# Kernel optimization log

Hardware: AMD Instinct MI355X
Metric: run time of the kernel (lower is better)

## Reference

```python
import jax, jax.numpy as jnp
import numpy as np
from jax import lax

EPS = 1e-5
B, T, H, L, K = 64, 1024, 12, 120, 5  # batch, seq len, hidden, lstm layers, conv kernel


def _init(key, shape, scale):
    return scale * jax.random.normal(key, shape, dtype=jnp.float32)


def setup_inputs() -> dict:
    key = jax.random.key(0)
    ks = jax.random.split(key, 16)
    return {
        "x": jax.random.normal(ks[0], (B, 6, T), dtype=jnp.float32),
        "conv_acc_w": _init(ks[1], (6, 6, K), 0.3),
        "conv_acc_b": jnp.zeros((6,), jnp.float32),
        "bn1_gamma": jnp.ones((6,), jnp.float32),
        "bn1_beta": jnp.zeros((6,), jnp.float32),
        "conv_ang_w": _init(ks[2], (6, 6, K), 0.3),
        "conv_ang_b": jnp.zeros((6,), jnp.float32),
        "bn2_gamma": jnp.ones((6,), jnp.float32),
        "bn2_beta": jnp.zeros((6,), jnp.float32),
        "attn_w": _init(ks[3], (H, 6), 0.4),
        "attn_b": jnp.zeros((H,), jnp.float32),
        "lstm_wih": _init(ks[4], (L, 4 * H, H), 0.2),
        "lstm_whh": _init(ks[5], (L, 4 * H, H), 0.2),
        "lstm_bih": _init(ks[6], (L, 4 * H), 0.1),
        "lstm_bhh": _init(ks[7], (L, 4 * H), 0.1),
        "lin1_w": _init(ks[8], (H, H), 0.3),
        "lin1_b": jnp.zeros((H,), jnp.float32),
        "lin2_w": _init(ks[9], (H, H), 0.3),
        "lin2_b": jnp.zeros((H,), jnp.float32),
        "mu_w": _init(ks[10], (H, H), 0.3),
        "mu_b": jnp.zeros((H,), jnp.float32),
        "sigma_w": _init(ks[11], (H, H), 0.3),
        "sigma_b": jnp.zeros((H,), jnp.float32),
    }


def _conv1d(x, w, b):
    # x: (B, C, T) valid conv, matches nn.Conv1d
    y = lax.conv_general_dilated(x, w, (1,), "VALID", dimension_numbers=("NCH", "OIH", "NCH"))
    return y + b[None, :, None]


def _batchnorm(x, gamma, beta):
    # training-mode BatchNorm1d: biased batch stats over (N, T)
    mean = jnp.mean(x, axis=(0, 2), keepdims=True)
    var = jnp.var(x, axis=(0, 2), keepdims=True)
    return (x - mean) * lax.rsqrt(var + EPS) * gamma[None, :, None] + beta[None, :, None]


def _lstm_stack(seq_tbh, wih, whh, bias):
    # seq_tbh: (T', B, H); stacked 120-layer LSTM, torch gate order (i, f, g, o)
    b = seq_tbh.shape[1]
    h0 = jnp.zeros((b, H), seq_tbh.dtype)

    def layer(seq, p):
        w_ih, w_hh, bb = p

        def step(carry, xt):
            h, c = carry
            g = xt @ w_ih.T + h @ w_hh.T + bb  # (B, 4H)
            i, f, gg, o = jnp.split(g, 4, axis=-1)
            c_new = jax.nn.sigmoid(f) * c + jax.nn.sigmoid(i) * jnp.tanh(gg)
            h_new = jax.nn.sigmoid(o) * jnp.tanh(c_new)
            return (h_new, c_new), h_new

        (h_T, _), out = lax.scan(step, (h0, h0), seq)
        return out, h_T

    _, h_last = lax.scan(layer, seq_tbh, (wih, whh, bias))
    return h_last  # (L, B, H): final hidden state of every layer


def _forward(x, conv_acc_w, conv_acc_b, bn1_gamma, bn1_beta, conv_ang_w, conv_ang_b,
             bn2_gamma, bn2_beta, attn_w, attn_b, lstm_wih, lstm_whh, lstm_bih, lstm_bhh,
             lin1_w, lin1_b, lin2_w, lin2_b, mu_w, mu_b, sigma_w, sigma_b):
    out_acc = jax.nn.relu(_batchnorm(_conv1d(x, conv_acc_w, conv_acc_b), bn1_gamma, bn1_beta))
    out_ang = jax.nn.relu(_batchnorm(_conv1d(out_acc, conv_ang_w, conv_ang_b), bn2_gamma, bn2_beta))
    feat = jax.nn.relu(jnp.einsum("bct,hc->bth", out_ang, attn_w) + attn_b)  # (B, T-8, H)
    seq = jnp.transpose(feat, (1, 0, 2))  # (T', B, H) time-major for scan
    h_last = _lstm_stack(seq, lstm_wih, lstm_whh, lstm_bih + lstm_bhh)
    h = jnp.transpose(h_last, (1, 0, 2))  # (B, L, H) == hidden_state.permute(1,0,2)
    h = jax.nn.relu(h @ lin1_w.T + lin1_b)
    out = jax.nn.relu(h @ lin2_w.T + lin2_b)
    mu = out @ mu_w.T + mu_b
    log_var = jax.nn.softplus(out @ sigma_w.T + sigma_b)
    return out, mu, log_var


def reference(x, conv_acc_w, conv_acc_b, bn1_gamma, bn1_beta, conv_ang_w, conv_ang_b,
              bn2_gamma, bn2_beta, attn_w, attn_b, lstm_wih, lstm_whh, lstm_bih, lstm_bhh,
              lin1_w, lin1_b, lin2_w, lin2_b, mu_w, mu_b, sigma_w, sigma_b):
    return _forward(x, conv_acc_w, conv_acc_b, bn1_gamma, bn1_beta, conv_ang_w, conv_ang_b,
                    bn2_gamma, bn2_beta, attn_w, attn_b, lstm_wih, lstm_whh, lstm_bih, lstm_bhh,
                    lin1_w, lin1_b, lin2_w, lin2_b, mu_w, mu_b, sigma_w, sigma_b)
```

## Files before the change

kernel.cpp:

```cpp
#include <hip/hip_runtime.h>
#include <math.h>

#define NLAY 120
#define TT   1016
#define NB   64
#define RB   8
#define IRS  32
#define TPB  384
#define BIGF (1 << 20)

typedef float v2f __attribute__((ext_vector_type(2)));

__device__ __forceinline__ float fast_rcp(float x) { return __builtin_amdgcn_rcpf(x); }
__device__ __forceinline__ float fast_sig(float x) { return fast_rcp(1.f + __expf(-x)); }
__device__ __forceinline__ float fast_tanh(float x) { return 1.f - 2.f * fast_rcp(1.f + __expf(2.f * x)); }

__device__ __forceinline__ int poll_ge_ag(const int* p, int tgt, int cur) {
  long g = 0;
  while (cur < tgt) {
    cur = __hip_atomic_load(p, __ATOMIC_RELAXED, __HIP_MEMORY_SCOPE_AGENT);
    if (cur >= tgt) break;
    __builtin_amdgcn_s_sleep(1);
    if (++g > 400000L) break;
  }
  return cur;
}
__device__ __forceinline__ int poll_ge_wg(const int* p, int tgt, int cur) {
  long g = 0;
  while (cur < tgt) {
    cur = __hip_atomic_load(p, __ATOMIC_RELAXED, __HIP_MEMORY_SCOPE_WORKGROUP);
    if (cur >= tgt) break;
    __builtin_amdgcn_s_sleep(1);
    if (++g > 400000L) break;
  }
  return cur;
}

__global__ void k_conv(const float* __restrict__ xin, const float* __restrict__ cw,
                       const float* __restrict__ cb, const float* __restrict__ aff,
                       float* __restrict__ yout, float* __restrict__ stat,
                       int Tin, int Tout, int use_aff)
{
  const int bx = blockIdx.x;
  const int b = bx / 6, co = bx - b * 6;
  const int tid = threadIdx.x;
  __shared__ float wsh[30];
  __shared__ float ssh[6], shsh[6];
  if (tid < 30) wsh[tid] = cw[co * 30 + tid];
  if (tid < 6) {
    ssh[tid]  = use_aff ? aff[tid] : 1.f;
    shsh[tid] = use_aff ? aff[6 + tid] : 0.f;
  }
  __syncthreads();
  const float bias = cb[co];
  float lsum = 0.f, lsq = 0.f;
  for (int t = tid; t < Tout; t += 256) {
    float acc = bias;
#pragma unroll
    for (int ci = 0; ci < 6; ++ci) {
      const float* xr = xin + ((size_t)b * 6 + ci) * Tin + t;
      const float s = ssh[ci], sh = shsh[ci];
#pragma unroll
      for (int k = 0; k < 5; ++k) {
        float v = xr[k];
        if (use_aff) v = fmaxf(fmaf(s, v, sh), 0.f);
        acc += wsh[ci * 5 + k] * v;
      }
    }
    yout[((size_t)b * 6 + co) * Tout + t] = acc;
    lsum += acc; lsq += acc * acc;
  }
  __shared__ float rs[256], rq[256];
  rs[tid] = lsum; rq[tid] = lsq;
  __syncthreads();
  for (int s = 128; s > 0; s >>= 1) {
    if (tid < s) { rs[tid] += rs[tid + s]; rq[tid] += rq[tid + s]; }
    __syncthreads();
  }
  if (tid == 0) { atomicAdd(&stat[co], rs[0]); atomicAdd(&stat[6 + co], rq[0]); }
}

__global__ void k_finalize(const float* __restrict__ stat,
                           const float* __restrict__ gamma, const float* __restrict__ beta,
                           float* __restrict__ aff, float invN)
{
  const int c = threadIdx.x;
  if (c < 6) {
    float mean = stat[c] * invN;
    float var  = stat[6 + c] * invN - mean * mean;
    float sc   = gamma[c] * rsqrtf(var + 1e-5f);
    aff[c]     = sc;
    aff[6 + c] = fmaf(-mean, sc, beta[c]);
  }
}

__global__ void k_attn(const float* __restrict__ y2, const float* __restrict__ aff2,
                       const float* __restrict__ aw, const float* __restrict__ ab,
                       float* __restrict__ seq0)
{
  const int t = blockIdx.x;
  const int tid = threadIdx.x;
  __shared__ float zb[6 * 64];
  if (tid < 384) {
    const int c = tid >> 6, bb = tid & 63;
    float v = y2[((size_t)bb * 6 + c) * TT + t];
    zb[c * 64 + bb] = fmaxf(fmaf(aff2[c], v, aff2[6 + c]), 0.f);
  }
  __syncthreads();
  const int b = tid / 12, j = tid - b * 12;
  float acc = ab[j];
#pragma unroll
  for (int c = 0; c < 6; ++c) acc += aw[j * 6 + c] * zb[c * 64 + b];
  seq0[(size_t)t * 768 + tid] = fmaxf(acc, 0.f);
}

__global__ __launch_bounds__(TPB, 2) void k_lstm(
    const float* __restrict__ wih, const float* __restrict__ whh,
    const float* __restrict__ bih, const float* __restrict__ bhh,
    const float* __restrict__ seq0, float* __restrict__ ring,
    int* __restrict__ prog, int* __restrict__ cons,
    float* __restrict__ hfin)
{
  const int bid  = blockIdx.x;
  const int c    = bid >> 2;
  const int seg  = bid & 3;
  const int tid  = threadIdx.x;
  const int w    = tid >> 6;
  const int lane = tid & 63;
  const int p    = lane / 12;
  const int j    = lane - p * 12;
  const bool act = (p < 5);
  const int pc   = act ? p : 0;
  const int l    = seg * 30 + w * 5 + pc;

  __shared__ __align__(16) float hloc[6][2][64];
  __shared__ __align__(16) float iring[5][IRS][12];
  __shared__ __align__(16) float xring[2][16][12];
  __shared__ __align__(16) float oring[16][12];
  __shared__ int pflag[6];
  __shared__ int cflag[8];
  float* xrf = &xring[0][0][0];

  if (tid < 6) pflag[tid] = 0;
  if (tid < 8) cflag[tid] = 0;
  hloc[w][0][lane] = 0.f; hloc[w][1][lane] = 0.f;
  __syncthreads();

  v2f wx_if[12], wx_go[12], wh_if[12], wh_go[12];
  v2f b_if = (v2f){0.f, 0.f}, b_go = (v2f){0.f, 0.f};
  if (act) {
    const float* wi = wih + l * 576;
    const float* wh = whh + l * 576;
#pragma unroll
    for (int k = 0; k < 12; ++k) {
      wx_if[k] = (v2f){ wi[(j     ) * 12 + k], wi[(j + 12) * 12 + k] };
      wx_go[k] = (v2f){ wi[(j + 24) * 12 + k], wi[(j + 36) * 12 + k] };
      wh_if[k] = (v2f){ wh[(j     ) * 12 + k], wh[(j + 12) * 12 + k] };
      wh_go[k] = (v2f){ wh[(j + 24) * 12 + k], wh[(j + 36) * 12 + k] };
    }
    const float* ba = bih + l * 48;
    const float* bb = bhh + l * 48;
    b_if = (v2f){ ba[j]      + bb[j],      ba[j + 12] + bb[j + 12] };
    b_go = (v2f){ ba[j + 24] + bb[j + 24], ba[j + 36] + bb[j + 36] };
  }

  const int hop_in  = c * 3 + seg - 1;
  const int hop_out = c * 3 + seg;
  const float* rin  = ring + (size_t)((seg > 0) ? hop_in : 0) * (RB * 192);
  float*       rout = ring + (size_t)((seg < 3) ? hop_out : 0) * (RB * 192);
  const bool is_feeder = (w == 0);
  const bool is_tailer = (w == 5) && (seg < 3);

  const int f0 = lane, f1 = lane + 64, f2 = lane + 128;
  const int s0o0 = (f0 / 12) * 768 + (f0 % 12);
  const int s0o1 = (f1 / 12) * 768 + (f1 % 12);
  const int s0o2 = (f2 / 12) * 768 + (f2 % 12);

  auto ld_batch = [&](int m, float* d) {
    if (seg == 0) {
      const float* b = seq0 + (size_t)m * 16 * 768 + c * 12;
      d[0] = b[s0o0]; d[1] = b[s0o1]; d[2] = b[s0o2];
    } else {
      const float* b = rin + (m & (RB - 1)) * 192;
      d[0] = __hip_atomic_load(b + f0, __ATOMIC_RELAXED, __HIP_MEMORY_SCOPE_AGENT);
      d[1] = __hip_atomic_load(b + f1, __ATOMIC_RELAXED, __HIP_MEMORY_SCOPE_AGENT);
      d[2] = __hip_atomic_load(b + f2, __ATOMIC_RELAXED, __HIP_MEMORY_SCOPE_AGENT);
    }
  };

  float pend[3] = {0.f, 0.f, 0.f};
  int kp = 0, kcons = 0;
  if (is_feeder) {
    if (seg > 0) kp = poll_ge_ag(&prog[hop_in], 2, 0);
    float cur[3];
    ld_batch(0, cur);
    ld_batch(1, pend);
    xrf[f0] = cur[0]; xrf[f1] = cur[1]; xrf[f2] = cur[2];
  }

  float cst = 0.f;
  int pcache = 0, ccache = 0;

  auto step = [&](int s, bool guard) __attribute__((always_inline)) {
    const int t  = s - pc;
    const int rb = (s & 1) ^ 1, wb = s & 1;

    const float* ax;
    if (p == 0) ax = (w == 0) ? (xrf + ((s >> 4) & 1) * 192 + (s & 15) * 12)
                              : (&iring[w - 1][s & (IRS - 1)][0]);
    else        ax = &hloc[w][rb][(pc == 0 ? 0 : pc - 1) * 12];
    const float* ah = &hloc[w][rb][pc * 12];

    float4 xA = ((const float4*)ax)[0], xB = ((const float4*)ax)[1], xC = ((const float4*)ax)[2];
    float4 hA = ((const float4*)ah)[0], hB = ((const float4*)ah)[1], hC = ((const float4*)ah)[2];
    float xv[12] = {xA.x,xA.y,xA.z,xA.w, xB.x,xB.y,xB.z,xB.w, xC.x,xC.y,xC.z,xC.w};
    float hv[12] = {hA.x,hA.y,hA.z,hA.w, hB.x,hB.y,hB.z,hB.w, hC.x,hC.y,hC.z,hC.w};

    v2f axif = (v2f){0.f,0.f}, axgo = (v2f){0.f,0.f};
    v2f ahif = b_if, ahgo = b_go;
#pragma unroll
    for (int k = 0; k < 12; ++k) {
      v2f xx = { xv[k], xv[k] };
      axif = __builtin_elementwise_fma(wx_if[k], xx, axif);
      axgo = __builtin_elementwise_fma(wx_go[k], xx, axgo);
    }
#pragma unroll
    for (int k = 0; k < 12; ++k) {
      v2f hh = { hv[k], hv[k] };
      ahif = __builtin_elementwise_fma(wh_if[k], hh, ahif);
      ahgo = __builtin_elementwise_fma(wh_go[k], hh, ahgo);
    }
    v2f aif = axif + ahif, ago = axgo + ahgo;
    float ig = fast_sig(aif.x);
    float fg = fast_sig(aif.y);
    float gg = fast_tanh(ago.x);
    float og = fast_sig(ago.y);

    if (!guard) {
      cst = fg * cst + ig * gg;
      float hn = og * fast_tanh(cst);
      hloc[w][wb][p * 12 + j] = hn;
      if (p == 4) {
        if (w < 5) iring[w][t & (IRS - 1)][j] = hn;
        else if (seg < 3) oring[t & 15][j] = hn;
      }
    } else {
      const bool run = act && (t >= 0) && (t < TT);
      if (run) {
        cst = fg * cst + ig * gg;
        float hn = og * fast_tanh(cst);
        hloc[w][wb][p * 12 + j] = hn;
        if (p == 4) {
          if (w < 5) iring[w][t & (IRS - 1)][j] = hn;
          else if (seg < 3) oring[t & 15][j] = hn;
        }
        if (t == TT - 1) hfin[l * 768 + c * 12 + j] = hn;
      }
    }

    if (is_tailer) {
      const int t4 = s - 4;
      if (t4 >= 0 && t4 < TT && (((t4 & 15) == 15) || t4 == TT - 1)) {
        const int m4 = t4 >> 4;
        if (kcons < m4 - (RB - 1) + 1)
          kcons = poll_ge_ag(&cons[hop_out], m4 - RB + 1, kcons);
        const float* orf = &oring[0][0];
        float o0 = orf[f0], o1 = orf[f1], o2 = orf[f2];
        float* d = rout + (m4 & (RB - 1)) * 192;
        __hip_atomic_store(d + f0, o0, __ATOMIC_RELAXED, __HIP_MEMORY_SCOPE_AGENT);
        __hip_atomic_store(d + f1, o1, __ATOMIC_RELAXED, __HIP_MEMORY_SCOPE_AGENT);
        __hip_atomic_store(d + f2, o2, __ATOMIC_RELAXED, __HIP_MEMORY_SCOPE_AGENT);
        if (lane == 0)
          __hip_atomic_store(&prog[hop_out], m4 + 1, __ATOMIC_RELEASE, __HIP_MEMORY_SCOPE_AGENT);
      }
    }
  };

  for (int s4 = 0; s4 < 1024; s4 += 4) {
    if (is_feeder && (s4 & 15) == 0) {
      const int m = s4 >> 4;
      if (m + 1 < NB) {
        float* xd = xrf + ((m + 1) & 1) * 192;
        xd[f0] = pend[0]; xd[f1] = pend[1]; xd[f2] = pend[2];
      }
      if (m + 2 < NB) {
        if (seg > 0 && kp < m + 3) kp = poll_ge_ag(&prog[hop_in], m + 3, kp);
        ld_batch(m + 2, pend);
      }
      if (seg > 0 && lane == 0)
        __hip_atomic_store(&cons[hop_in], m, __ATOMIC_RELAXED, __HIP_MEMORY_SCOPE_AGENT);
    }

    if (w > 0 && s4 < TT) {
      const int tgt = (s4 + 4 < TT) ? (s4 + 4) : TT;
      if (pcache < tgt) {
        pcache = poll_ge_wg(&pflag[w - 1], tgt, pcache);
        asm volatile("" ::: "memory");
      }
    }
    if (w < 5 && s4 >= 36) {
      const int tgt = s4 - 32;
      if (ccache < tgt) {
        ccache = poll_ge_wg(&cflag[w + 1], tgt, ccache);
        asm volatile("" ::: "memory");
      }
    }

    if (s4 >= 4 && s4 < 1012) {
      step(s4 + 0, false); step(s4 + 1, false); step(s4 + 2, false); step(s4 + 3, false);
    } else {
      step(s4 + 0, true);  step(s4 + 1, true);  step(s4 + 2, true);  step(s4 + 3, true);
    }

    if (lane == 0) {
      asm volatile("" ::: "memory");
      if (w < 5)
        __hip_atomic_store(&pflag[w], s4, __ATOMIC_RELAXED, __HIP_MEMORY_SCOPE_WORKGROUP);
      if (w > 0 && s4 + 3 < TT)
        __hip_atomic_store(&cflag[w], s4 + 4, __ATOMIC_RELAXED, __HIP_MEMORY_SCOPE_WORKGROUP);
    }
  }

  if (lane == 0) {
    asm volatile("" ::: "memory");
    if (w < 5) __hip_atomic_store(&pflag[w], BIGF, __ATOMIC_RELAXED, __HIP_MEMORY_SCOPE_WORKGROUP);
    if (w > 0) __hip_atomic_store(&cflag[w], BIGF, __ATOMIC_RELAXED, __HIP_MEMORY_SCOPE_WORKGROUP);
    if (is_feeder && seg > 0)
      __hip_atomic_store(&cons[hop_in], BIGF, __ATOMIC_RELAXED, __HIP_MEMORY_SCOPE_AGENT);
  }
}

__global__ void k_head(const float* __restrict__ hfin,
                       const float* __restrict__ w1, const float* __restrict__ b1,
                       const float* __restrict__ w2, const float* __restrict__ b2,
                       const float* __restrict__ wm, const float* __restrict__ bm,
                       const float* __restrict__ wsg, const float* __restrict__ bsg,
                       float* __restrict__ out)
{
  const int tid = threadIdx.x;
  __shared__ float s1[144], s2[144], sm[144], ss[144];
  __shared__ float v1[12], v2[12], vm[12], vs[12];
  if (tid < 144) { s1[tid] = w1[tid]; s2[tid] = w2[tid]; sm[tid] = wm[tid]; ss[tid] = wsg[tid]; }
  if (tid < 12)  { v1[tid] = b1[tid]; v2[tid] = b2[tid]; vm[tid] = bm[tid]; vs[tid] = bsg[tid]; }
  __syncthreads();
  const int r = blockIdx.x * 256 + tid;
  const int b = r / 120, l = r - b * 120;
  float h[12];
#pragma unroll
  for (int k = 0; k < 12; ++k) h[k] = hfin[l * 768 + b * 12 + k];
  float u1[12];
#pragma unroll
  for (int u = 0; u < 12; ++u) {
    float a = v1[u];
#pragma unroll
    for (int k = 0; k < 12; ++k) a += s1[u * 12 + k] * h[k];
    u1[u] = fmaxf(a, 0.f);
  }
  float u2[12];
#pragma unroll
  for (int u = 0; u < 12; ++u) {
    float a = v2[u];
#pragma unroll
    for (int k = 0; k < 12; ++k) a += s2[u * 12 + k] * u1[k];
    u2[u] = fmaxf(a, 0.f);
  }
  const size_t base = (size_t)r * 12;
#pragma unroll
  for (int u = 0; u < 12; ++u) out[base + u] = u2[u];
#pragma unroll
  for (int u = 0; u < 12; ++u) {
    float a = vm[u];
#pragma unroll
    for (int k = 0; k < 12; ++k) a += sm[u * 12 + k] * u2[k];
    out[92160 + base + u] = a;
  }
#pragma unroll
  for (int u = 0; u < 12; ++u) {
    float a = vs[u];
#pragma unroll
    for (int k = 0; k < 12; ++k) a += ss[u * 12 + k] * u2[k];
    out[184320 + base + u] = fmaxf(a, 0.f) + log1pf(expf(-fabsf(a)));
  }
}

extern "C" void kernel_launch(void* const* d_in, const int* in_sizes, int n_in,
                              void* d_out, int out_size, void* d_ws, size_t ws_size,
                              hipStream_t stream)
{
  const float* x   = (const float*)d_in[0];
  const float* c1w = (const float*)d_in[1];
  const float* c1b = (const float*)d_in[2];
  const float* g1  = (const float*)d_in[3];
  const float* be1 = (const float*)d_in[4];
  const float* c2w = (const float*)d_in[5];
  const float* c2b = (const float*)d_in[6];
  const float* g2  = (const float*)d_in[7];
  const float* be2 = (const float*)d_in[8];
  const float* aw  = (const float*)d_in[9];
  const float* ab  = (const float*)d_in[10];
  const float* wih = (const float*)d_in[11];
  const float* whh = (const float*)d_in[12];
  const float* bih = (const float*)d_in[13];
  const float* bhh = (const float*)d_in[14];
  const float* l1w = (const float*)d_in[15];
  const float* l1b = (const float*)d_in[16];
  const float* l2w = (const float*)d_in[17];
  const float* l2b = (const float*)d_in[18];
  const float* muw = (const float*)d_in[19];
  const float* mub = (const float*)d_in[20];
  const float* sgw = (const float*)d_in[21];
  const float* sgb = (const float*)d_in[22];

  float* ws    = (float*)d_ws;
  float* stat1 = ws;
  float* stat2 = ws + 12;
  float* aff1  = ws + 24;
  float* aff2  = ws + 36;
  int*   prog  = (int*)(ws + 64);
  int*   cons  = (int*)(ws + 304);
  float* y1    = ws + 576;
  float* y2    = y1 + 391680;
  float* seq0  = y2 + 390144;
  float* ring  = seq0 + 780288;
  float* hfin  = ring + (size_t)192 * RB * 192;

  hipMemsetAsync(d_ws, 0, 576 * sizeof(float), stream);

  k_conv<<<384, 256, 0, stream>>>(x, c1w, c1b, nullptr, y1, stat1, 1024, 1020, 0);
  k_finalize<<<1, 64, 0, stream>>>(stat1, g1, be1, aff1, 1.f / 65280.f);
  k_conv<<<384, 256, 0, stream>>>(y1, c2w, c2b, aff1, y2, stat2, 1020, 1016, 1);
  k_finalize<<<1, 64, 0, stream>>>(stat2, g2, be2, aff2, 1.f / 65024.f);
  k_attn<<<1016, 768, 0, stream>>>(y2, aff2, aw, ab, seq0);
  k_lstm<<<256, TPB, 0, stream>>>(wih, whh, bih, bhh, seq0, ring, prog, cons, hfin);
  k_head<<<30, 256, 0, stream>>>(hfin, l1w, l1b, l2w, l2b, muw, mub, sgw, sgb, (float*)d_out);
}
```

Measured before the change: 811.2 us.

## Process two batch chains per LSTM block with reorganized weight layout and batched flushes

Each LSTM workgroup now runs two batch columns (chains A and B) at once, so half as many blocks are launched and every weight register is reused for two independent recurrences. Gate weights are regrouped into per-gate rows with paired k elements, which lets the input vectors feed packed FMAs directly without broadcasting. The step loop is unrolled by 8 instead of 4, intra-block flag syncs are coarsened, and the output ring flush moves from per-step inside the tail wave to a separate double-buffered flush. The intent is to interleave two dependency chains to hide latency and halve synchronization overhead per sample, at the cost of more registers and LDS per block, and fewer blocks to spread across CUs.

```diff
diff --git a/kernel.cpp b/kernel.cpp
--- a/kernel.cpp
+++ b/kernel.cpp
@@ -7,7 +7,6 @@
 #define RB   8
 #define IRS  32
 #define TPB  384
-#define BIGF (1 << 20)
 
 typedef float v2f __attribute__((ext_vector_type(2)));
 
@@ -122,8 +121,9 @@
     float* __restrict__ hfin)
 {
   const int bid  = blockIdx.x;
-  const int c    = bid >> 2;
+  const int cb   = bid >> 2;
   const int seg  = bid & 3;
+  const int cA   = cb * 2, cB = cb * 2 + 1;
   const int tid  = threadIdx.x;
   const int w    = tid >> 6;
   const int lane = tid & 63;
@@ -133,52 +133,52 @@
   const int pc   = act ? p : 0;
   const int l    = seg * 30 + w * 5 + pc;
 
-  __shared__ __align__(16) float hloc[6][2][64];
-  __shared__ __align__(16) float iring[5][IRS][12];
-  __shared__ __align__(16) float xring[2][16][12];
-  __shared__ __align__(16) float oring[16][12];
-  __shared__ int pflag[6];
-  __shared__ int cflag[8];
-  float* xrf = &xring[0][0][0];
-
-  if (tid < 6) pflag[tid] = 0;
-  if (tid < 8) cflag[tid] = 0;
-  hloc[w][0][lane] = 0.f; hloc[w][1][lane] = 0.f;
+  __shared__ __align__(16) float hlocA[6][2][64], hlocB[6][2][64];
+  __shared__ __align__(16) float iringA[5][IRS][12], iringB[5][IRS][12];
+  __shared__ __align__(16) float xrA[2][192], xrB[2][192];
+  __shared__ __align__(16) float obA[2][192], obB[2][192];
+  __shared__ int pflag[8], cflag[8];
+
+  if (tid < 8) { pflag[tid] = 0; cflag[tid] = 0; }
+  hlocA[w][0][lane] = 0.f; hlocA[w][1][lane] = 0.f;
+  hlocB[w][0][lane] = 0.f; hlocB[w][1][lane] = 0.f;
   __syncthreads();
 
-  v2f wx_if[12], wx_go[12], wh_if[12], wh_go[12];
-  v2f b_if = (v2f){0.f, 0.f}, b_go = (v2f){0.f, 0.f};
+  v2f wx[4][6] = {}, wh2[4][6] = {};
+  float bias[4] = {0.f, 0.f, 0.f, 0.f};
   if (act) {
     const float* wi = wih + l * 576;
     const float* wh = whh + l * 576;
 #pragma unroll
-    for (int k = 0; k < 12; ++k) {
-      wx_if[k] = (v2f){ wi[(j     ) * 12 + k], wi[(j + 12) * 12 + k] };
-      wx_go[k] = (v2f){ wi[(j + 24) * 12 + k], wi[(j + 36) * 12 + k] };
-      wh_if[k] = (v2f){ wh[(j     ) * 12 + k], wh[(j + 12) * 12 + k] };
-      wh_go[k] = (v2f){ wh[(j + 24) * 12 + k], wh[(j + 36) * 12 + k] };
-    }
-    const float* ba = bih + l * 48;
-    const float* bb = bhh + l * 48;
-    b_if = (v2f){ ba[j]      + bb[j],      ba[j + 12] + bb[j + 12] };
-    b_go = (v2f){ ba[j + 24] + bb[j + 24], ba[j + 36] + bb[j + 36] };
-  }
-
-  const int hop_in  = c * 3 + seg - 1;
-  const int hop_out = c * 3 + seg;
-  const float* rin  = ring + (size_t)((seg > 0) ? hop_in : 0) * (RB * 192);
-  float*       rout = ring + (size_t)((seg < 3) ? hop_out : 0) * (RB * 192);
+    for (int q = 0; q < 4; ++q) {
+      const int row = j + 12 * q;
+#pragma unroll
+      for (int kk = 0; kk < 6; ++kk) {
+        wx[q][kk]  = *(const v2f*)(wi + row * 12 + 2 * kk);
+        wh2[q][kk] = *(const v2f*)(wh + row * 12 + 2 * kk);
+      }
+      bias[q] = bih[l * 48 + row] + bhh[l * 48 + row];
+    }
+  }
+
+  const int hopAi = cA * 3 + seg - 1, hopBi = cB * 3 + seg - 1;
+  const int hopAo = cA * 3 + seg,     hopBo = cB * 3 + seg;
+  const bool has_up = (seg > 0), has_dn = (seg < 3);
+  const float* rinA = ring + (size_t)(has_up ? hopAi : 0) * (RB * 192);
+  const float* rinB = ring + (size_t)(has_up ? hopBi : 0) * (RB * 192);
+  float* routA = ring + (size_t)(has_dn ? hopAo : 0) * (RB * 192);
+  float* routB = ring + (size_t)(has_dn ? hopBo : 0) * (RB * 192);
   const bool is_feeder = (w == 0);
-  const bool is_tailer = (w == 5) && (seg < 3);
+  const bool is_tailer = (w == 5) && has_dn;
 
   const int f0 = lane, f1 = lane + 64, f2 = lane + 128;
   const int s0o0 = (f0 / 12) * 768 + (f0 % 12);
   const int s0o1 = (f1 / 12) * 768 + (f1 % 12);
   const int s0o2 = (f2 / 12) * 768 + (f2 % 12);
 
-  auto ld_batch = [&](int m, float* d) {
+  auto ld_batch = [&](int m, const float* rin, int chain, float* d) {
     if (seg == 0) {
-      const float* b = seq0 + (size_t)m * 16 * 768 + c * 12;
+      const float* b = seq0 + (size_t)m * 16 * 768 + chain * 12;
       d[0] = b[s0o0]; d[1] = b[s0o1]; d[2] = b[s0o2];
     } else {
       const float* b = rin + (m & (RB - 1)) * 192;
@@ -188,146 +188,183 @@
     }
   };
 
-  float pend[3] = {0.f, 0.f, 0.f};
-  int kp = 0, kcons = 0;
+  float pendA[3] = {0,0,0}, pendB[3] = {0,0,0};
+  int kpA = 0, kpB = 0, kcA = 0, kcB = 0;
   if (is_feeder) {
-    if (seg > 0) kp = poll_ge_ag(&prog[hop_in], 2, 0);
-    float cur[3];
-    ld_batch(0, cur);
-    ld_batch(1, pend);
-    xrf[f0] = cur[0]; xrf[f1] = cur[1]; xrf[f2] = cur[2];
-  }
-
-  float cst = 0.f;
+    if (has_up) { kpA = poll_ge_ag(&prog[hopAi], 2, 0); kpB = poll_ge_ag(&prog[hopBi], 2, 0); }
+    float curA[3], curB[3];
+    ld_batch(0, rinA, cA, curA); ld_batch(0, rinB, cB, curB);
+    xrA[0][f0] = curA[0]; xrA[0][f1] = curA[1]; xrA[0][f2] = curA[2];
+    xrB[0][f0] = curB[0]; xrB[0][f1] = curB[1]; xrB[0][f2] = curB[2];
+    ld_batch(1, rinA, cA, pendA); ld_batch(1, rinB, cB, pendB);
+  }
+
+  float cstA = 0.f, hnA = 0.f, cstB = 0.f, hnB = 0.f;
   int pcache = 0, ccache = 0;
 
   auto step = [&](int s, bool guard) __attribute__((always_inline)) {
-    const int t  = s - pc;
     const int rb = (s & 1) ^ 1, wb = s & 1;
-
-    const float* ax;
-    if (p == 0) ax = (w == 0) ? (xrf + ((s >> 4) & 1) * 192 + (s & 15) * 12)
-                              : (&iring[w - 1][s & (IRS - 1)][0]);
-    else        ax = &hloc[w][rb][(pc == 0 ? 0 : pc - 1) * 12];
-    const float* ah = &hloc[w][rb][pc * 12];
-
-    float4 xA = ((const float4*)ax)[0], xB = ((const float4*)ax)[1], xC = ((const float4*)ax)[2];
-    float4 hA = ((const float4*)ah)[0], hB = ((const float4*)ah)[1], hC = ((const float4*)ah)[2];
-    float xv[12] = {xA.x,xA.y,xA.z,xA.w, xB.x,xB.y,xB.z,xB.w, xC.x,xC.y,xC.z,xC.w};
-    float hv[12] = {hA.x,hA.y,hA.z,hA.w, hB.x,hB.y,hB.z,hB.w, hC.x,hC.y,hC.z,hC.w};
-
-    v2f axif = (v2f){0.f,0.f}, axgo = (v2f){0.f,0.f};
-    v2f ahif = b_if, ahgo = b_go;
-#pragma unroll
-    for (int k = 0; k < 12; ++k) {
-      v2f xx = { xv[k], xv[k] };
-      axif = __builtin_elementwise_fma(wx_if[k], xx, axif);
-      axgo = __builtin_elementwise_fma(wx_go[k], xx, axgo);
-    }
-#pragma unroll
-    for (int k = 0; k < 12; ++k) {
-      v2f hh = { hv[k], hv[k] };
-      ahif = __builtin_elementwise_fma(wh_if[k], hh, ahif);
-      ahgo = __builtin_elementwise_fma(wh_go[k], hh, ahgo);
-    }
-    v2f aif = axif + ahif, ago = axgo + ahgo;
-    float ig = fast_sig(aif.x);
-    float fg = fast_sig(aif.y);
-    float gg = fast_tanh(ago.x);
-    float og = fast_sig(ago.y);
+    const float* bxA;
+    const float* bxB;
+    if (p == 0) {
+      if (w == 0) { bxA = &xrA[(s >> 4) & 1][(s & 15) * 12]; bxB = &xrB[(s >> 4) & 1][(s & 15) * 12]; }
+      else        { bxA = &iringA[w - 1][s & (IRS - 1)][0];  bxB = &iringB[w - 1][s & (IRS - 1)][0]; }
+    } else {
+      bxA = &hlocA[w][rb][(pc ? pc - 1 : 0) * 12];
+      bxB = &hlocB[w][rb][(pc ? pc - 1 : 0) * 12];
+    }
+    const float* bhA = &hlocA[w][rb][pc * 12];
+    const float* bhB = &hlocB[w][rb][pc * 12];
+    float4 xA0=((const float4*)bxA)[0], xA1=((const float4*)bxA)[1], xA2=((const float4*)bxA)[2];
+    float4 hA0=((const float4*)bhA)[0], hA1=((const float4*)bhA)[1], hA2=((const float4*)bhA)[2];
+    float4 xB0=((const float4*)bxB)[0], xB1=((const float4*)bxB)[1], xB2=((const float4*)bxB)[2];
+    float4 hB0=((const float4*)bhB)[0], hB1=((const float4*)bhB)[1], hB2=((const float4*)bhB)[2];
+    v2f pxA[6]={{xA0.x,xA0.y},{xA0.z,xA0.w},{xA1.x,xA1.y},{xA1.z,xA1.w},{xA2.x,xA2.y},{xA2.z,xA2.w}};
+    v2f phA[6]={{hA0.x,hA0.y},{hA0.z,hA0.w},{hA1.x,hA1.y},{hA1.z,hA1.w},{hA2.x,hA2.y},{hA2.z,hA2.w}};
+    v2f pxB[6]={{xB0.x,xB0.y},{xB0.z,xB0.w},{xB1.x,xB1.y},{xB1.z,xB1.w},{xB2.x,xB2.y},{xB2.z,xB2.w}};
+    v2f phB[6]={{hB0.x,hB0.y},{hB0.z,hB0.w},{hB1.x,hB1.y},{hB1.z,hB1.w},{hB2.x,hB2.y},{hB2.z,hB2.w}};
+
+    v2f aA0={bias[0],0.f}, aA1={bias[1],0.f}, aA2={bias[2],0.f}, aA3={bias[3],0.f};
+    v2f aB0={bias[0],0.f}, aB1={bias[1],0.f}, aB2={bias[2],0.f}, aB3={bias[3],0.f};
+#pragma unroll
+    for (int kk = 0; kk < 6; ++kk) {
+      aA0 = __builtin_elementwise_fma(wx[0][kk], pxA[kk], aA0);
+      aB0 = __builtin_elementwise_fma(wx[0][kk], pxB[kk], aB0);
+      aA1 = __builtin_elementwise_fma(wx[1][kk], pxA[kk], aA1);
+      aB1 = __builtin_elementwise_fma(wx[1][kk], pxB[kk], aB1);
+      aA2 = __builtin_elementwise_fma(wx[2][kk], pxA[kk], aA2);
+      aB2 = __builtin_elementwise_fma(wx[2][kk], pxB[kk], aB2);
+      aA3 = __builtin_elementwise_fma(wx[3][kk], pxA[kk], aA3);
+      aB3 = __builtin_elementwise_fma(wx[3][kk], pxB[kk], aB3);
+    }
+#pragma unroll
+    for (int kk = 0; kk < 6; ++kk) {
+      aA0 = __builtin_elementwise_fma(wh2[0][kk], phA[kk], aA0);
+      aB0 = __builtin_elementwise_fma(wh2[0][kk], phB[kk], aB0);
+      aA1 = __builtin_elementwise_fma(wh2[1][kk], phA[kk], aA1);
+      aB1 = __builtin_elementwise_fma(wh2[1][kk], phB[kk], aB1);
+      aA2 = __builtin_elementwise_fma(wh2[2][kk], phA[kk], aA2);
+      aB2 = __builtin_elementwise_fma(wh2[2][kk], phB[kk], aB2);
+      aA3 = __builtin_elementwise_fma(wh2[3][kk], phA[kk], aA3);
+      aB3 = __builtin_elementwise_fma(wh2[3][kk], phB[kk], aB3);
+    }
+    float igA = fast_sig(aA0.x + aA0.y), igB = fast_sig(aB0.x + aB0.y);
+    float fgA = fast_sig(aA1.x + aA1.y), fgB = fast_sig(aB1.x + aB1.y);
+    float gvA = fast_tanh(aA2.x + aA2.y), gvB = fast_tanh(aB2.x + aB2.y);
+    float ogA = fast_sig(aA3.x + aA3.y), ogB = fast_sig(aB3.x + aB3.y);
 
     if (!guard) {
-      cst = fg * cst + ig * gg;
-      float hn = og * fast_tanh(cst);
-      hloc[w][wb][p * 12 + j] = hn;
+      cstA = fgA * cstA + igA * gvA;  cstB = fgB * cstB + igB * gvB;
+      hnA  = ogA * fast_tanh(cstA);   hnB  = ogB * fast_tanh(cstB);
+      hlocA[w][wb][lane] = hnA;       hlocB[w][wb][lane] = hnB;
       if (p == 4) {
-        if (w < 5) iring[w][t & (IRS - 1)][j] = hn;
-        else if (seg < 3) oring[t & 15][j] = hn;
+        const int t = s - 4;
+        if (w < 5) { iringA[w][t & (IRS - 1)][j] = hnA; iringB[w][t & (IRS - 1)][j] = hnB; }
+        else if (has_dn) {
+          obA[(t >> 4) & 1][(t & 15) * 12 + j] = hnA;
+          obB[(t >> 4) & 1][(t & 15) * 12 + j] = hnB;
+        }
       }
     } else {
+      const int t = s - pc;
       const bool run = act && (t >= 0) && (t < TT);
       if (run) {
-        cst = fg * cst + ig * gg;
-        float hn = og * fast_tanh(cst);
-        hloc[w][wb][p * 12 + j] = hn;
-        if (p == 4) {
-          if (w < 5) iring[w][t & (IRS - 1)][j] = hn;
-          else if (seg < 3) oring[t & 15][j] = hn;
+        cstA = fgA * cstA + igA * gvA;  cstB = fgB * cstB + igB * gvB;
+        hnA  = ogA * fast_tanh(cstA);   hnB  = ogB * fast_tanh(cstB);
+      }
+      hlocA[w][wb][lane] = hnA; hlocB[w][wb][lane] = hnB;
+      if (p == 4 && t >= 0 && t < TT) {
+        if (w < 5) { iringA[w][t & (IRS - 1)][j] = hnA; iringB[w][t & (IRS - 1)][j] = hnB; }
+        else if (has_dn) {
+          obA[(t >> 4) & 1][(t & 15) * 12 + j] = hnA;
+          obB[(t >> 4) & 1][(t & 15) * 12 + j] = hnB;
         }
-        if (t == TT - 1) hfin[l * 768 + c * 12 + j] = hn;
-      }
-    }
-
-    if (is_tailer) {
-      const int t4 = s - 4;
-      if (t4 >= 0 && t4 < TT && (((t4 & 15) == 15) || t4 == TT - 1)) {
-        const int m4 = t4 >> 4;
-        if (kcons < m4 - (RB - 1) + 1)
-          kcons = poll_ge_ag(&cons[hop_out], m4 - RB + 1, kcons);
-        const float* orf = &oring[0][0];
-        float o0 = orf[f0], o1 = orf[f1], o2 = orf[f2];
-        float* d = rout + (m4 & (RB - 1)) * 192;
-        __hip_atomic_store(d + f0, o0, __ATOMIC_RELAXED, __HIP_MEMORY_SCOPE_AGENT);
-        __hip_atomic_store(d + f1, o1, __ATOMIC_RELAXED, __HIP_MEMORY_SCOPE_AGENT);
-        __hip_atomic_store(d + f2, o2, __ATOMIC_RELAXED, __HIP_MEMORY_SCOPE_AGENT);
-        if (lane == 0)
-          __hip_atomic_store(&prog[hop_out], m4 + 1, __ATOMIC_RELEASE, __HIP_MEMORY_SCOPE_AGENT);
-      }
-    }
+      }
+      if (run && t == TT - 1) {
+        hfin[l * 768 + cA * 12 + j] = hnA;
+        hfin[l * 768 + cB * 12 + j] = hnB;
+      }
+    }
+    __builtin_amdgcn_wave_barrier();
   };
 
-  for (int s4 = 0; s4 < 1024; s4 += 4) {
-    if (is_feeder && (s4 & 15) == 0) {
-      const int m = s4 >> 4;
+  auto flush = [&](int b) {
+    if (kcA < b - (RB - 1)) kcA = poll_ge_ag(&cons[hopAo], b - (RB - 1), kcA);
+    if (kcB < b - (RB - 1)) kcB = poll_ge_ag(&cons[hopBo], b - (RB - 1), kcB);
+    const float* oa = &obA[b & 1][0];
+    const float* ob = &obB[b & 1][0];
+    float a0 = oa[f0], a1 = oa[f1], a2 = oa[f2];
+    float b0 = ob[f0], b1 = ob[f1], b2 = ob[f2];
+    float* dA = routA + (b & (RB - 1)) * 192;
+    float* dB = routB + (b & (RB - 1)) * 192;
+    __hip_atomic_store(dA + f0, a0, __ATOMIC_RELAXED, __HIP_MEMORY_SCOPE_AGENT);
+    __hip_atomic_store(dA + f1, a1, __ATOMIC_RELAXED, __HIP_MEMORY_SCOPE_AGENT);
+    __hip_atomic_store(dA + f2, a2, __ATOMIC_RELAXED, __HIP_MEMORY_SCOPE_AGENT);
+    __hip_atomic_store(dB + f0, b0, __ATOMIC_RELAXED, __HIP_MEMORY_SCOPE_AGENT);
+    __hip_atomic_store(dB + f1, b1, __ATOMIC_RELAXED, __HIP_MEMORY_SCOPE_AGENT);
+    __hip_atomic_store(dB + f2, b2, __ATOMIC_RELAXED, __HIP_MEMORY_SCOPE_AGENT);
+    if (lane == 0) {
+      __hip_atomic_store(&prog[hopAo], b + 1, __ATOMIC_RELEASE, __HIP_MEMORY_SCOPE_AGENT);
+      __hip_atomic_store(&prog[hopBo], b + 1, __ATOMIC_RELEASE, __HIP_MEMORY_SCOPE_AGENT);
+    }
+  };
+
+  for (int s8 = 0; s8 < 1024; s8 += 8) {
+    if (is_feeder && (s8 & 15) == 0) {
+      const int m = s8 >> 4;
       if (m + 1 < NB) {
-        float* xd = xrf + ((m + 1) & 1) * 192;
-        xd[f0] = pend[0]; xd[f1] = pend[1]; xd[f2] = pend[2];
+        float* xa = &xrA[(m + 1) & 1][0];
+        float* xb = &xrB[(m + 1) & 1][0];
+        xa[f0] = pendA[0]; xa[f1] = pendA[1]; xa[f2] = pendA[2];
+        xb[f0] = pendB[0]; xb[f1] = pendB[1]; xb[f2] = pendB[2];
+      }
+      if (has_up && lane == 0) {
+        __hip_atomic_store(&cons[hopAi], m, __ATOMIC_RELAXED, __HIP_MEMORY_SCOPE_AGENT);
+        __hip_atomic_store(&cons[hopBi], m, __ATOMIC_RELAXED, __HIP_MEMORY_SCOPE_AGENT);
       }
       if (m + 2 < NB) {
-        if (seg > 0 && kp < m + 3) kp = poll_ge_ag(&prog[hop_in], m + 3, kp);
-        ld_batch(m + 2, pend);
-      }
-      if (seg > 0 && lane == 0)
-        __hip_atomic_store(&cons[hop_in], m, __ATOMIC_RELAXED, __HIP_MEMORY_SCOPE_AGENT);
-    }
-
-    if (w > 0 && s4 < TT) {
-      const int tgt = (s4 + 4 < TT) ? (s4 + 4) : TT;
+        if (has_up) {
+          const int tgt = (m + 3 < NB) ? m + 3 : NB;
+          if (kpA < tgt) kpA = poll_ge_ag(&prog[hopAi], tgt, kpA);
+          if (kpB < tgt) kpB = poll_ge_ag(&prog[hopBi], tgt, kpB);
+        }
+        ld_batch(m + 2, rinA, cA, pendA);
+        ld_batch(m + 2, rinB, cB, pendB);
+      }
+    }
+    if (is_tailer && (s8 & 15) == 8 && s8 >= 24) flush((s8 - 24) >> 4);
+
+    if (w > 0) {
+      const int tgt = (s8 + 12 < 1020) ? s8 + 12 : 1020;
       if (pcache < tgt) {
         pcache = poll_ge_wg(&pflag[w - 1], tgt, pcache);
         asm volatile("" ::: "memory");
       }
     }
-    if (w < 5 && s4 >= 36) {
-      const int tgt = s4 - 32;
+    if (w < 5 && s8 >= 32) {
+      const int tgt = s8 - 24;
       if (ccache < tgt) {
         ccache = poll_ge_wg(&cflag[w + 1], tgt, ccache);
         asm volatile("" ::: "memory");
       }
     }
 
-    if (s4 >= 4 && s4 < 1012) {
-      step(s4 + 0, false); step(s4 + 1, false); step(s4 + 2, false); step(s4 + 3, false);
+    if (s8 >= 8 && s8 < 1008) {
+      step(s8 + 0, false); step(s8 + 1, false); step(s8 + 2, false); step(s8 + 3, false);
+      step(s8 + 4, false); step(s8 + 5, false); step(s8 + 6, false); step(s8 + 7, false);
     } else {
-      step(s4 + 0, true);  step(s4 + 1, true);  step(s4 + 2, true);  step(s4 + 3, true);
+      step(s8 + 0, true);  step(s8 + 1, true);  step(s8 + 2, true);  step(s8 + 3, true);
+      step(s8 + 4, true);  step(s8 + 5, true);  step(s8 + 6, true);  step(s8 + 7, true);
     }
 
     if (lane == 0) {
       asm volatile("" ::: "memory");
-      if (w < 5)
-        __hip_atomic_store(&pflag[w], s4, __ATOMIC_RELAXED, __HIP_MEMORY_SCOPE_WORKGROUP);
-      if (w > 0 && s4 + 3 < TT)
-        __hip_atomic_store(&cflag[w], s4 + 4, __ATOMIC_RELAXED, __HIP_MEMORY_SCOPE_WORKGROUP);
-    }
-  }
-
-  if (lane == 0) {
-    asm volatile("" ::: "memory");
-    if (w < 5) __hip_atomic_store(&pflag[w], BIGF, __ATOMIC_RELAXED, __HIP_MEMORY_SCOPE_WORKGROUP);
-    if (w > 0) __hip_atomic_store(&cflag[w], BIGF, __ATOMIC_RELAXED, __HIP_MEMORY_SCOPE_WORKGROUP);
-    if (is_feeder && seg > 0)
-      __hip_atomic_store(&cons[hop_in], BIGF, __ATOMIC_RELAXED, __HIP_MEMORY_SCOPE_AGENT);
-  }
+      if (w < 5) __hip_atomic_store(&pflag[w], s8 + 8, __ATOMIC_RELAXED, __HIP_MEMORY_SCOPE_WORKGROUP);
+      if (w > 0) __hip_atomic_store(&cflag[w], s8 + 8, __ATOMIC_RELAXED, __HIP_MEMORY_SCOPE_WORKGROUP);
+    }
+  }
+
+  if (is_tailer) flush(NB - 1);
 }
 
 __global__ void k_head(const float* __restrict__ hfin,
@@ -431,6 +468,6 @@
   k_conv<<<384, 256, 0, stream>>>(y1, c2w, c2b, aff1, y2, stat2, 1020, 1016, 1);
   k_finalize<<<1, 64, 0, stream>>>(stat2, g2, be2, aff2, 1.f / 65024.f);
   k_attn<<<1016, 768, 0, stream>>>(y2, aff2, aw, ab, seq0);
-  k_lstm<<<256, TPB, 0, stream>>>(wih, whh, bih, bhh, seq0, ring, prog, cons, hfin);
+  k_lstm<<<128, TPB, 0, stream>>>(wih, whh, bih, bhh, seq0, ring, prog, cons, hfin);
   k_head<<<30, 256, 0, stream>>>(hfin, l1w, l1b, l2w, l2b, muw, mub, sgw, sgb, (float*)d_out);
 }
```

Result: slower. 1.360 ms (+67.7%).
